# Optimization experiments

Hardware: AMD Instinct MI355X
Metric: run time of the kernel (lower is better)

## Reference

```python
import jax, jax.numpy as jnp
import numpy as np


def setup_inputs() -> dict:
    key = jax.random.key(0)
    k1, k2, k3, k4 = jax.random.split(key, 4)
    n, c, p1, p2, r = 8, 3, 512, 512, 8
    X = jax.random.uniform(k1, (n, c, p1, p2), dtype=jnp.float32)
    S = jax.random.uniform(k2, (c, r), dtype=jnp.float32)
    S = S / (jnp.linalg.norm(S, axis=0, keepdims=True))  # unit-norm columns like S_init
    gamma = jax.random.uniform(k3, (1,), dtype=jnp.float32) * 1e-05
    lam = jax.random.uniform(k4, (1,), dtype=jnp.float32) * 1e-05
    return {"X": X, "S": S, "gamma": gamma, "lam": lam, "n_iter": 2}


def reference(X, S, gamma, lam, n_iter):
    n, c, p1, p2 = X.shape
    p = p1 * p2
    r = S.shape[1]
    Xf = X.reshape(n, c, p)
    gamma = jnp.abs(gamma)
    lam = jnp.abs(lam)
    Dt = jnp.zeros((n, r, p), dtype=X.dtype)
    x0 = jnp.mean(Xf, axis=2, keepdims=True)
    for _ in range(n_iter):
        # ---- D update (proximal gradient) ----
        SDt = jnp.einsum('cr,nrp->ncp', S, Dt)  # S @ Dt
        x0 = jnp.mean(Xf + SDt, axis=2, keepdims=True)  # [n,c,1]
        tau_D = 1.0 / jnp.sum(S * S)  # 1/||S||_F^2
        Dt = Dt - tau_D * jnp.einsum('cr,ncp->nrp', S, SDt + Xf - x0)
        S_nrm = jnp.linalg.norm(S, axis=0).reshape(1, r, 1)  # [1,r,1]
        Dt = jax.nn.relu(Dt - lam * gamma * tau_D * S_nrm)
        Dt_L2 = jnp.linalg.norm(Dt, axis=2, keepdims=True)  # [n,r,1]
        scl = jax.nn.relu(Dt_L2 - lam * tau_D * S_nrm)
        scl = scl / Dt_L2 + 1e-10  # faithful to source (eps added after divide)
        Dt = Dt * scl
        # ---- S update (proximal gradient) ----
        SDt = jnp.einsum('cr,nrp->ncp', S, Dt)
        x0 = jnp.mean(Xf + SDt, axis=2, keepdims=True)
        Dt_sum = jnp.sum(Dt, axis=2, keepdims=True)  # [n,r,1]
        tau_S = 1.0 / jnp.mean(jnp.sum(Dt * Dt, axis=(1, 2)))
        grad = jnp.mean(
            jnp.einsum('ncp,nqp->ncq', SDt + Xf, Dt)
            - x0 @ jnp.transpose(Dt_sum, (0, 2, 1)),
            axis=0)  # [c,r]
        S_grad = S - tau_S * grad
        Dt_nrm = jnp.mean(
            gamma * jnp.sum(jnp.abs(Dt), axis=2, keepdims=True)
            + jnp.linalg.norm(Dt, axis=2, keepdims=True), axis=0)  # [r,1]
        Sg_nrm = jnp.linalg.norm(S_grad, axis=0, keepdims=True)  # [1,r]
        scl_S = jax.nn.relu(Sg_nrm - lam * tau_S * Dt_nrm.T)
        scl_S = scl_S / (Sg_nrm + 1e-10)
        S = S_grad * scl_S
        # ---- unit-norm rescale (unit_norm_S=True) ----
        S_nrm2 = jnp.linalg.norm(S, axis=0, keepdims=True)  # [1,r]
        S = S / (S_nrm2 + 1e-10)
        Dt = Dt * (S_nrm2.reshape(1, r, 1) + 1e-10)
    return x0, S, Dt.reshape(n, r, p1, p2)
```

## Files before the change

kernel.cpp:

```cpp
#include <hip/hip_runtime.h>

constexpr int N = 8, C = 3, R = 8;
constexpr int P = 512 * 512;
constexpr int BLK = 256;
constexpr int NB = 64;
constexpr int PPB = P / NB;
constexpr int PITER = PPB / (BLK * 4);
constexpr int NK = 68;

typedef float f32x4 __attribute__((ext_vector_type(4)));

constexpr int W_XMEAN = 0;
constexpr int W_S1    = 32;
constexpr int W_F1    = 64;
constexpr int W_THR2  = 128;
constexpr int W_TAU2  = 136;
constexpr int W_SNRM2 = 144;
constexpr int W_X02   = 160;
constexpr int W_PXF   = 256;
constexpr int W_PA    = 2048;
constexpr int W_PB    = 36864;

#define XR8(M) M(0) M(1) M(2) M(3) M(4) M(5) M(6) M(7)
#define XTRI(M) \
  M(0,0) \
  M(1,0) M(1,1) \
  M(2,0) M(2,1) M(2,2) \
  M(3,0) M(3,1) M(3,2) M(3,3) \
  M(4,0) M(4,1) M(4,2) M(4,3) M(4,4) \
  M(5,0) M(5,1) M(5,2) M(5,3) M(5,4) M(5,5) \
  M(6,0) M(6,1) M(6,2) M(6,3) M(6,4) M(6,5) M(6,6) \
  M(7,0) M(7,1) M(7,2) M(7,3) M(7,4) M(7,5) M(7,6) M(7,7)
#define XCR(M) \
  M(0,0) M(0,1) M(0,2) M(0,3) M(0,4) M(0,5) M(0,6) M(0,7) \
  M(1,0) M(1,1) M(1,2) M(1,3) M(1,4) M(1,5) M(1,6) M(1,7) \
  M(2,0) M(2,1) M(2,2) M(2,3) M(2,4) M(2,5) M(2,6) M(2,7)

__device__ __forceinline__ float sld(float x) {
    return __uint_as_float(__builtin_amdgcn_readfirstlane(__float_as_uint(x)));
}
__device__ __forceinline__ float waveSum(float v) {
    #pragma unroll
    for (int o = 32; o > 0; o >>= 1) v += __shfl_down(v, o);
    return v;
}

__global__ __launch_bounds__(BLK)
void k_xmean(const float* __restrict__ X, float* __restrict__ ws) {
    int nc = blockIdx.y;
    int t = threadIdx.x;
    size_t base = (size_t)nc * P + (size_t)blockIdx.x * 4096;
    float s = 0.f;
    #pragma unroll
    for (int i = 0; i < 4; ++i) {
        float4 q = *(const float4*)(X + base + (size_t)(i * BLK + t) * 4);
        s += (q.x + q.y) + (q.z + q.w);
    }
    __shared__ float red[4];
    s = waveSum(s);
    int lane = t & 63, wid = t >> 6;
    if (lane == 0) red[wid] = s;
    __syncthreads();
    if (t == 0) ws[W_PXF + nc * 64 + blockIdx.x] = (red[0] + red[1]) + (red[2] + red[3]);
}

template <int IT>
__device__ void t23_math(const float* __restrict__ redL, const float* __restrict__ Sin,
                         const float* __restrict__ ws, float lam_, float gam_,
                         float* oS, float* oF, float* oTH2, float* oTAU2,
                         float* oX02, float* oSN2, float* ox0s) {
    const int t = threadIdx.x;
    __shared__ float sum_[N][R], T_[N][R][R], U_[N][C][R];
    __shared__ float scl_[N][R], L2_[N][R], x0s_[N][C], dtn_[R];
    __shared__ float Scur_[24], grad_[24], snrm_in[8];
    __shared__ float tauS_, tauD_;
    for (int i = t; i < NK * N; i += BLK) {
        int k = i / N, nn = i % N;
        float v = redL[k * N + nn];
        if (k < 8) sum_[nn][k] = v;
        else if (k < 44) {
            int m = k - 8; int q = 0;
            while ((q + 1) * (q + 2) / 2 <= m) ++q;
            int r = m - q * (q + 1) / 2;
            T_[nn][r][q] = v; T_[nn][q][r] = v;
        } else { int m = k - 44; U_[nn][m >> 3][m & 7] = v; }
    }
    if (t < 24) Scur_[t] = IT ? ws[W_S1 + t] : Sin[t];
    if (t == 0) {
        if (IT) tauD_ = ws[W_TAU2];
        else { float s = 0.f; for (int i = 0; i < 24; ++i) s += Sin[i] * Sin[i]; tauD_ = 1.0f / s; }
    }
    if (t < 8) {
        if (IT) snrm_in[t] = ws[W_SNRM2 + t];
        else snrm_in[t] = sqrtf(Sin[t] * Sin[t] + Sin[8 + t] * Sin[8 + t] + Sin[16 + t] * Sin[16 + t]);
    }
    __syncthreads();
    for (int i = t; i < N * C * R; i += BLK) {
        int nn = i / 24, m = i % 24, c = m >> 3, q = m & 7;
        U_[nn][c][q] += ws[W_XMEAN + nn * 3 + c] * sum_[nn][q];
    }
    if (t < 64) {
        int nn = t >> 3, r = t & 7;
        float l2 = sqrtf(T_[nn][r][r]);
        float scl = fmaxf(l2 - lam_ * tauD_ * snrm_in[r], 0.f) / l2 + 1e-10f;
        scl_[nn][r] = scl; L2_[nn][r] = l2;
    }
    __syncthreads();
    if (t == 0) {
        float tot = 0.f;
        for (int nn = 0; nn < N; ++nn)
            for (int r = 0; r < R; ++r)
                tot += scl_[nn][r] * scl_[nn][r] * T_[nn][r][r];
        tauS_ = (float)N / tot;
    }
    if (t < 24) {
        int nn = t / 3, c = t % 3;
        float acc = ws[W_XMEAN + t];
        #pragma unroll
        for (int r = 0; r < R; ++r)
            acc += Scur_[c * R + r] * scl_[nn][r] * sum_[nn][r] * (1.0f / P);
        x0s_[nn][c] = acc;
        if (IT == 1) ox0s[t] = acc;
    }
    if (t >= 32 && t < 40) {
        int r = t - 32;
        float a = 0.f;
        #pragma unroll
        for (int nn = 0; nn < N; ++nn)
            a += scl_[nn][r] * (gam_ * sum_[nn][r] + L2_[nn][r]);
        dtn_[r] = a * (1.0f / N);
    }
    __syncthreads();
    if (t < 24) {
        int c = t / 8, q = t % 8;
        float a = 0.f;
        #pragma unroll
        for (int nn = 0; nn < N; ++nn) {
            float m = U_[nn][c][q];
            #pragma unroll
            for (int r = 0; r < R; ++r)
                m += Scur_[c * R + r] * scl_[nn][r] * T_[nn][r][q];
            a += scl_[nn][q] * (m - x0s_[nn][c] * sum_[nn][q]);
        }
        grad_[t] = a * (1.0f / N);
    }
    __syncthreads();
    if (t == 0) {
        float Sg[24], Sn[24];
        #pragma unroll
        for (int i = 0; i < 24; ++i) Sg[i] = Scur_[i] - tauS_ * grad_[i];
        #pragma unroll
        for (int q = 0; q < 8; ++q) {
            float s2 = 0.f;
            #pragma unroll
            for (int c = 0; c < 3; ++c) s2 += Sg[c * 8 + q] * Sg[c * 8 + q];
            float sgn = sqrtf(s2);
            float s = fmaxf(sgn - lam_ * tauS_ * dtn_[q], 0.f) / (sgn + 1e-10f);
            #pragma unroll
            for (int c = 0; c < 3; ++c) Sn[c * 8 + q] = Sg[c * 8 + q] * s;
        }
        #pragma unroll
        for (int q = 0; q < 8; ++q) {
            float s2 = 0.f;
            #pragma unroll
            for (int c = 0; c < 3; ++c) s2 += Sn[c * 8 + q] * Sn[c * 8 + q];
            float n2 = sqrtf(s2);
            oSN2[q] = n2;
            #pragma unroll
            for (int c = 0; c < 3; ++c) oS[c * 8 + q] = Sn[c * 8 + q] / (n2 + 1e-10f);
        }
        if (IT == 0) {
            float ssq = 0.f;
            #pragma unroll
            for (int i = 0; i < 24; ++i) ssq += oS[i] * oS[i];
            float tau2 = 1.0f / ssq;
            oTAU2[0] = tau2;
            #pragma unroll
            for (int r = 0; r < 8; ++r) {
                float s2 = oS[r] * oS[r] + oS[8 + r] * oS[8 + r] + oS[16 + r] * oS[16 + r];
                oTH2[r] = lam_ * gam_ * tau2 * sqrtf(s2);
            }
        }
    }
    __syncthreads();
    if (t < 64) oF[t] = scl_[t >> 3][t & 7] * (oSN2[t & 7] + 1e-10f);
    __syncthreads();
    if (IT == 0 && t < 24) {
        int nn = t / 3, c = t % 3;
        float acc = ws[W_XMEAN + t];
        #pragma unroll
        for (int r = 0; r < R; ++r)
            acc += oS[c * R + r] * oF[nn * R + r] * sum_[nn][r] * (1.0f / P);
        oX02[t] = acc;
    }
    __syncthreads();
}

template <int MODE>
__global__ __launch_bounds__(BLK, 1)
void k_dpass(const float* __restrict__ X, const float* __restrict__ Sin,
             const float* __restrict__ gp, const float* __restrict__ lp,
             float* __restrict__ ws, const float* __restrict__ part_in,
             float* __restrict__ part_out, float* __restrict__ Dt_out,
             float* __restrict__ x0_out, float* __restrict__ S_out) {
    const int n = blockIdx.y, t = threadIdx.x;

    __shared__ float redL[NK * N];
    __shared__ float oS[24], oF[64], oTH2[8], oTAU2[1], oX02[24], oSN2[8], ox0s[24];
    __shared__ float Lxm[24];
    __shared__ float redE[4 * NK];

    const float lamv = fabsf(*lp), gamv = fabsf(*gp);

    float ssq0 = 0.f;
    #pragma unroll
    for (int i = 0; i < 24; ++i) { float v = Sin[i]; ssq0 = fmaf(v, v, ssq0); }
    const float tau1c = sld(1.0f / ssq0);
#define LD_TH1(r) const float th1_##r = sld(lamv * gamv * tau1c * sqrtf(fmaf(Sin[r], Sin[r], fmaf(Sin[8 + r], Sin[8 + r], Sin[16 + r] * Sin[16 + r]))));
    XR8(LD_TH1)

    if constexpr (MODE == 0) {
        if (t < 24) {
            const float* px = ws + W_PXF + t * 64;
            float s = 0.f;
            #pragma unroll
            for (int j = 0; j < 64; ++j) s += px[j];
            Lxm[t] = s * (1.0f / P);
        }
        __syncthreads();
        if (blockIdx.x == 0 && n == 0 && t < 24) ws[W_XMEAN + t] = Lxm[t];
    } else {
        for (int row = t; row < NK * N; row += BLK) {
            const float* pr = part_in + (size_t)row * NB;
            float s = 0.f;
            #pragma unroll
            for (int j = 0; j < NB / 4; ++j) {
                float4 q = *(const float4*)(pr + j * 4);
                s += (q.x + q.y) + (q.z + q.w);
            }
            redL[row] = s;
        }
        __syncthreads();
        t23_math<(MODE == 1 ? 0 : 1)>(redL, Sin, ws, lamv, gamv,
                                      oS, oF, oTH2, oTAU2, oX02, oSN2, ox0s);
        if constexpr (MODE == 1) {
            if (blockIdx.x == 0 && n == 0) {
                if (t < 24) ws[W_S1 + t] = oS[t];
                if (t < 64) ws[W_F1 + t] = oF[t];
                if (t < 8)  ws[W_THR2 + t] = oTH2[t];
                if (t == 0) ws[W_TAU2] = oTAU2[0];
                if (t < 24) ws[W_X02 + t] = oX02[t];
                if (t < 8)  ws[W_SNRM2 + t] = oSN2[t];
            }
        } else {
            if (blockIdx.x == 0 && n == 0 && t < 24) {
                x0_out[t] = ox0s[t];
                S_out[t] = oS[t];
            }
        }
    }

    const float x01_0 = sld(MODE == 0 ? Lxm[n * 3 + 0] : ws[W_XMEAN + n * 3 + 0]);
    const float x01_1 = sld(MODE == 0 ? Lxm[n * 3 + 1] : ws[W_XMEAN + n * 3 + 1]);
    const float x01_2 = sld(MODE == 0 ? Lxm[n * 3 + 2] : ws[W_XMEAN + n * 3 + 2]);
#define LD_S0(c,q) const float S0_##c##q = sld(Sin[(c) * 8 + (q)]);
    XCR(LD_S0)
#define LD_S1(c,q) const float S1_##c##q = (MODE >= 1) ? sld(MODE == 1 ? oS[(c) * 8 + (q)] : ws[W_S1 + (c) * 8 + (q)]) : 0.f;
    XCR(LD_S1)
#define LD_F1(r)  const float f1_##r = (MODE >= 1) ? sld(MODE == 1 ? oF[n * 8 + (r)] : ws[W_F1 + n * 8 + (r)]) : 0.f;
#define LD_TH2(r) const float th2_##r = (MODE >= 1) ? sld(MODE == 1 ? oTH2[(r)] : ws[W_THR2 + (r)]) : 0.f;
#define LD_F2(r)  const float f2_##r = (MODE == 2) ? sld(oF[n * 8 + (r)]) : 0.f;
    XR8(LD_F1) XR8(LD_TH2) XR8(LD_F2)
    const float tau2c = (MODE >= 1) ? sld(MODE == 1 ? oTAU2[0] : ws[W_TAU2]) : 0.f;
    const float dx0_0 = (MODE >= 1) ? sld(ws[W_XMEAN + n * 3 + 0] - (MODE == 1 ? oX02[n * 3 + 0] : ws[W_X02 + n * 3 + 0])) : 0.f;
    const float dx0_1 = (MODE >= 1) ? sld(ws[W_XMEAN + n * 3 + 1] - (MODE == 1 ? oX02[n * 3 + 1] : ws[W_X02 + n * 3 + 1])) : 0.f;
    const float dx0_2 = (MODE >= 1) ? sld(ws[W_XMEAN + n * 3 + 2] - (MODE == 1 ? oX02[n * 3 + 2] : ws[W_X02 + n * 3 + 2])) : 0.f;

#define D_SM(r)   float sm_##r = 0.f;
#define D_T(q,r)  float tq_##q##_##r = 0.f;
#define D_V(c,q)  float vv_##c##_##q = 0.f;
    XR8(D_SM) XTRI(D_T) XCR(D_V)

    const float* Xn = X + (size_t)n * C * P;
    float* Dn = Dt_out + (size_t)n * R * P;

#define C_P1(r) const float p_##r = fmaxf(fmaf(-tau1c, fmaf(S0_0##r, tt0, fmaf(S0_1##r, tt1, S0_2##r * tt2)), -th1_##r), 0.f);
#define C_AL(r) const float a_##r = p_##r;
#define C_D2(r) const float d_##r = f1_##r * p_##r;
#define C_W(c)  const float w##c = fmaf(S1_##c##0, d_0, fmaf(S1_##c##1, d_1, fmaf(S1_##c##2, d_2, fmaf(S1_##c##3, d_3, fmaf(S1_##c##4, d_4, fmaf(S1_##c##5, d_5, fmaf(S1_##c##6, d_6, fmaf(S1_##c##7, d_7, tt##c + dx0_##c))))))));
#define C_A2(r) const float a_##r = fmaxf(fmaf(-tau2c, fmaf(S1_0##r, w0, fmaf(S1_1##r, w1, S1_2##r * w2)), d_##r - th2_##r), 0.f);
#define AC_SM(r)  sm_##r += a_##r;
#define AC_T(q,r) tq_##q##_##r = fmaf(a_##r, a_##q, tq_##q##_##r);
#define AC_V(c,q) vv_##c##_##q = fmaf(tt##c, a_##q, vv_##c##_##q);
#define PXc(r) ov_##r.x = f2_##r * a_##r;
#define PYc(r) ov_##r.y = f2_##r * a_##r;
#define PZc(r) ov_##r.z = f2_##r * a_##r;
#define PWc(r) ov_##r.w = f2_##r * a_##r;
#define GXc(q) (q).x
#define GYc(q) (q).y
#define GZc(q) (q).z
#define GWc(q) (q).w

#define SITE(GET, PUTM) { \
    const float tt0 = GET(xv0) - x01_0; \
    const float tt1 = GET(xv1) - x01_1; \
    const float tt2 = GET(xv2) - x01_2; \
    XR8(C_P1) \
    if constexpr (MODE == 0) { \
        XR8(C_AL) XR8(AC_SM) XTRI(AC_T) XCR(AC_V) \
    } else { \
        XR8(C_D2) C_W(0) C_W(1) C_W(2) XR8(C_A2) \
        if constexpr (MODE == 1) { XR8(AC_SM) XTRI(AC_T) XCR(AC_V) } \
        else { XR8(PUTM) } \
    } }

#define D_OV(r) float4 ov_##r;
#define ST_O(r) { f32x4 wv = { ov_##r.x, ov_##r.y, ov_##r.z, ov_##r.w }; \
                  __builtin_nontemporal_store(wv, (f32x4*)(Dn + (size_t)(r) * P + pbase)); }

    #pragma unroll
    for (int it = 0; it < PITER; ++it) {
        size_t pbase = (size_t)blockIdx.x * PPB + (size_t)(it * BLK + t) * 4;
        float4 xv0 = *(const float4*)(Xn + 0 * (size_t)P + pbase);
        float4 xv1 = *(const float4*)(Xn + 1 * (size_t)P + pbase);
        float4 xv2 = *(const float4*)(Xn + 2 * (size_t)P + pbase);
        XR8(D_OV)
        SITE(GXc, PXc)
        SITE(GYc, PYc)
        SITE(GZc, PZc)
        SITE(GWc, PWc)
        if constexpr (MODE == 2) { XR8(ST_O) }
    }

    if constexpr (MODE < 2) {
        const int lane = t & 63, wid = t >> 6;
#define RD_SM(r)  { float v = waveSum(sm_##r);       if (lane == 0) redE[wid * NK + (r)] = v; }
#define RD_T(q,r) { float v = waveSum(tq_##q##_##r); if (lane == 0) redE[wid * NK + 8 + (q) * ((q) + 1) / 2 + (r)] = v; }
#define RD_V(c,q) { float v = waveSum(vv_##c##_##q); if (lane == 0) redE[wid * NK + 44 + (c) * R + (q)] = v; }
        XR8(RD_SM) XTRI(RD_T) XCR(RD_V)
        __syncthreads();
        for (int k = t; k < NK; k += BLK)
            part_out[((size_t)k * N + n) * NB + blockIdx.x] =
                (redE[k] + redE[NK + k]) + (redE[2 * NK + k] + redE[3 * NK + k]);
    }
}

extern "C" void kernel_launch(void* const* d_in, const int* in_sizes, int n_in,
                              void* d_out, int out_size, void* d_ws, size_t ws_size,
                              hipStream_t stream) {
    const float* X   = (const float*)d_in[0];
    const float* Sin = (const float*)d_in[1];
    const float* gam = (const float*)d_in[2];
    const float* lam = (const float*)d_in[3];
    float* out    = (float*)d_out;
    float* x0_out = out;
    float* S_out  = out + 24;
    float* Dt_out = out + 48;
    float* ws     = (float*)d_ws;
    float* partA  = ws + W_PA;
    float* partB  = ws + W_PB;

    k_xmean<<<dim3(64, N * C), BLK, 0, stream>>>(X, ws);
    k_dpass<0><<<dim3(NB, N), BLK, 0, stream>>>(X, Sin, gam, lam, ws, partA, partA, Dt_out, x0_out, S_out);
    k_dpass<1><<<dim3(NB, N), BLK, 0, stream>>>(X, Sin, gam, lam, ws, partA, partB, Dt_out, x0_out, S_out);
    k_dpass<2><<<dim3(NB, N), BLK, 0, stream>>>(X, Sin, gam, lam, ws, partB, partA, Dt_out, x0_out, S_out);
}
```

Baseline: 98.40 us.

## Replace partial-sum buffers with atomic accumulation and double block count

Cross-block reductions (the X means and the 68 per-batch statistics) now go through float atomicAdd into a small zeroed workspace instead of per-block partial arrays that every block re-reduced at the start of the next pass. Each block of MODE 2 recomputes the iteration-1 scalar math redundantly rather than reading it back from workspace. The grid doubles to 128 blocks per batch, and the in-block reduction uses quad shuffles plus a padded shared table. This removes the per-block partial re-read, at the cost of atomic contention, a memset launch, nondeterministic summation order and duplicated t23 math in MODE 2.

```diff
diff --git a/kernel.cpp b/kernel.cpp
--- a/kernel.cpp
+++ b/kernel.cpp
@@ -3,23 +3,17 @@
 constexpr int N = 8, C = 3, R = 8;
 constexpr int P = 512 * 512;
 constexpr int BLK = 256;
-constexpr int NB = 64;
+constexpr int NB = 128;
 constexpr int PPB = P / NB;
 constexpr int PITER = PPB / (BLK * 4);
 constexpr int NK = 68;
 
 typedef float f32x4 __attribute__((ext_vector_type(4)));
 
-constexpr int W_XMEAN = 0;
-constexpr int W_S1    = 32;
-constexpr int W_F1    = 64;
-constexpr int W_THR2  = 128;
-constexpr int W_TAU2  = 136;
-constexpr int W_SNRM2 = 144;
-constexpr int W_X02   = 160;
-constexpr int W_PXF   = 256;
-constexpr int W_PA    = 2048;
-constexpr int W_PB    = 36864;
+constexpr int W_XSUM = 0;
+constexpr int W_ACC1 = 32;
+constexpr int W_ACC2 = 608;
+constexpr int W_ZEND = 1152;
 
 #define XR8(M) M(0) M(1) M(2) M(3) M(4) M(5) M(6) M(7)
 #define XTRI(M) \
@@ -61,22 +55,25 @@
     int lane = t & 63, wid = t >> 6;
     if (lane == 0) red[wid] = s;
     __syncthreads();
-    if (t == 0) ws[W_PXF + nc * 64 + blockIdx.x] = (red[0] + red[1]) + (red[2] + red[3]);
+    if (t == 0) atomicAdd(ws + W_XSUM + nc, (red[0] + red[1]) + (red[2] + red[3]));
 }
 
 template <int IT>
-__device__ void t23_math(const float* __restrict__ redL, const float* __restrict__ Sin,
-                         const float* __restrict__ ws, float lam_, float gam_,
+__device__ void t23_math(const float* __restrict__ accG, const float* __restrict__ SinG,
+                         const float* __restrict__ iS, const float* __restrict__ iTau,
+                         const float* __restrict__ iCN, const float* __restrict__ ws,
+                         float lam_, float gam_,
                          float* oS, float* oF, float* oTH2, float* oTAU2,
-                         float* oX02, float* oSN2, float* ox0s) {
+                         float* oCN, float* oX02, float* ox0s) {
     const int t = threadIdx.x;
+    const float invP = 1.0f / (float)P;
     __shared__ float sum_[N][R], T_[N][R][R], U_[N][C][R];
     __shared__ float scl_[N][R], L2_[N][R], x0s_[N][C], dtn_[R];
-    __shared__ float Scur_[24], grad_[24], snrm_in[8];
+    __shared__ float Scur_[24], grad_[24], snrmI[8], pn_[8];
     __shared__ float tauS_, tauD_;
     for (int i = t; i < NK * N; i += BLK) {
         int k = i / N, nn = i % N;
-        float v = redL[k * N + nn];
+        float v = accG[i];
         if (k < 8) sum_[nn][k] = v;
         else if (k < 44) {
             int m = k - 8; int q = 0;
@@ -85,24 +82,24 @@
             T_[nn][r][q] = v; T_[nn][q][r] = v;
         } else { int m = k - 44; U_[nn][m >> 3][m & 7] = v; }
     }
-    if (t < 24) Scur_[t] = IT ? ws[W_S1 + t] : Sin[t];
+    if (t < 24) Scur_[t] = IT ? iS[t] : SinG[t];
     if (t == 0) {
-        if (IT) tauD_ = ws[W_TAU2];
-        else { float s = 0.f; for (int i = 0; i < 24; ++i) s += Sin[i] * Sin[i]; tauD_ = 1.0f / s; }
+        if (IT) tauD_ = iTau[0];
+        else { float s = 0.f; for (int i = 0; i < 24; ++i) s += SinG[i] * SinG[i]; tauD_ = 1.0f / s; }
     }
     if (t < 8) {
-        if (IT) snrm_in[t] = ws[W_SNRM2 + t];
-        else snrm_in[t] = sqrtf(Sin[t] * Sin[t] + Sin[8 + t] * Sin[8 + t] + Sin[16 + t] * Sin[16 + t]);
+        if (IT) snrmI[t] = iCN[t];
+        else snrmI[t] = sqrtf(SinG[t] * SinG[t] + SinG[8 + t] * SinG[8 + t] + SinG[16 + t] * SinG[16 + t]);
     }
     __syncthreads();
     for (int i = t; i < N * C * R; i += BLK) {
         int nn = i / 24, m = i % 24, c = m >> 3, q = m & 7;
-        U_[nn][c][q] += ws[W_XMEAN + nn * 3 + c] * sum_[nn][q];
+        U_[nn][c][q] += ws[W_XSUM + nn * 3 + c] * invP * sum_[nn][q];
     }
     if (t < 64) {
         int nn = t >> 3, r = t & 7;
         float l2 = sqrtf(T_[nn][r][r]);
-        float scl = fmaxf(l2 - lam_ * tauD_ * snrm_in[r], 0.f) / l2 + 1e-10f;
+        float scl = fmaxf(l2 - lam_ * tauD_ * snrmI[r], 0.f) / l2 + 1e-10f;
         scl_[nn][r] = scl; L2_[nn][r] = l2;
     }
     __syncthreads();
@@ -115,10 +112,10 @@
     }
     if (t < 24) {
         int nn = t / 3, c = t % 3;
-        float acc = ws[W_XMEAN + t];
+        float acc = ws[W_XSUM + t] * invP;
         #pragma unroll
         for (int r = 0; r < R; ++r)
-            acc += Scur_[c * R + r] * scl_[nn][r] * sum_[nn][r] * (1.0f / P);
+            acc += Scur_[c * R + r] * scl_[nn][r] * sum_[nn][r] * invP;
         x0s_[nn][c] = acc;
         if (IT == 1) ox0s[t] = acc;
     }
@@ -165,7 +162,7 @@
             #pragma unroll
             for (int c = 0; c < 3; ++c) s2 += Sn[c * 8 + q] * Sn[c * 8 + q];
             float n2 = sqrtf(s2);
-            oSN2[q] = n2;
+            pn_[q] = n2;
             #pragma unroll
             for (int c = 0; c < 3; ++c) oS[c * 8 + q] = Sn[c * 8 + q] / (n2 + 1e-10f);
         }
@@ -177,20 +174,21 @@
             oTAU2[0] = tau2;
             #pragma unroll
             for (int r = 0; r < 8; ++r) {
-                float s2 = oS[r] * oS[r] + oS[8 + r] * oS[8 + r] + oS[16 + r] * oS[16 + r];
-                oTH2[r] = lam_ * gam_ * tau2 * sqrtf(s2);
+                float cn = sqrtf(oS[r] * oS[r] + oS[8 + r] * oS[8 + r] + oS[16 + r] * oS[16 + r]);
+                oCN[r] = cn;
+                oTH2[r] = lam_ * gam_ * tau2 * cn;
             }
         }
     }
     __syncthreads();
-    if (t < 64) oF[t] = scl_[t >> 3][t & 7] * (oSN2[t & 7] + 1e-10f);
+    if (t < 64) oF[t] = scl_[t >> 3][t & 7] * (pn_[t & 7] + 1e-10f);
     __syncthreads();
     if (IT == 0 && t < 24) {
         int nn = t / 3, c = t % 3;
-        float acc = ws[W_XMEAN + t];
+        float acc = ws[W_XSUM + t] * invP;
         #pragma unroll
         for (int r = 0; r < R; ++r)
-            acc += oS[c * R + r] * oF[nn * R + r] * sum_[nn][r] * (1.0f / P);
+            acc += oS[c * R + r] * oF[nn * R + r] * sum_[nn][r] * invP;
         oX02[t] = acc;
     }
     __syncthreads();
@@ -200,17 +198,11 @@
 __global__ __launch_bounds__(BLK, 1)
 void k_dpass(const float* __restrict__ X, const float* __restrict__ Sin,
              const float* __restrict__ gp, const float* __restrict__ lp,
-             float* __restrict__ ws, const float* __restrict__ part_in,
-             float* __restrict__ part_out, float* __restrict__ Dt_out,
+             float* __restrict__ ws, float* __restrict__ Dt_out,
              float* __restrict__ x0_out, float* __restrict__ S_out) {
     const int n = blockIdx.y, t = threadIdx.x;
-
-    __shared__ float redL[NK * N];
-    __shared__ float oS[24], oF[64], oTH2[8], oTAU2[1], oX02[24], oSN2[8], ox0s[24];
-    __shared__ float Lxm[24];
-    __shared__ float redE[4 * NK];
-
     const float lamv = fabsf(*lp), gamv = fabsf(*gp);
+    const float invP = 1.0f / (float)P;
 
     float ssq0 = 0.f;
     #pragma unroll
@@ -219,62 +211,34 @@
 #define LD_TH1(r) const float th1_##r = sld(lamv * gamv * tau1c * sqrtf(fmaf(Sin[r], Sin[r], fmaf(Sin[8 + r], Sin[8 + r], Sin[16 + r] * Sin[16 + r]))));
     XR8(LD_TH1)
 
-    if constexpr (MODE == 0) {
-        if (t < 24) {
-            const float* px = ws + W_PXF + t * 64;
-            float s = 0.f;
-            #pragma unroll
-            for (int j = 0; j < 64; ++j) s += px[j];
-            Lxm[t] = s * (1.0f / P);
-        }
-        __syncthreads();
-        if (blockIdx.x == 0 && n == 0 && t < 24) ws[W_XMEAN + t] = Lxm[t];
-    } else {
-        for (int row = t; row < NK * N; row += BLK) {
-            const float* pr = part_in + (size_t)row * NB;
-            float s = 0.f;
-            #pragma unroll
-            for (int j = 0; j < NB / 4; ++j) {
-                float4 q = *(const float4*)(pr + j * 4);
-                s += (q.x + q.y) + (q.z + q.w);
-            }
-            redL[row] = s;
-        }
-        __syncthreads();
-        t23_math<(MODE == 1 ? 0 : 1)>(redL, Sin, ws, lamv, gamv,
-                                      oS, oF, oTH2, oTAU2, oX02, oSN2, ox0s);
-        if constexpr (MODE == 1) {
-            if (blockIdx.x == 0 && n == 0) {
-                if (t < 24) ws[W_S1 + t] = oS[t];
-                if (t < 64) ws[W_F1 + t] = oF[t];
-                if (t < 8)  ws[W_THR2 + t] = oTH2[t];
-                if (t == 0) ws[W_TAU2] = oTAU2[0];
-                if (t < 24) ws[W_X02 + t] = oX02[t];
-                if (t < 8)  ws[W_SNRM2 + t] = oSN2[t];
-            }
-        } else {
-            if (blockIdx.x == 0 && n == 0 && t < 24) {
-                x0_out[t] = ox0s[t];
-                S_out[t] = oS[t];
-            }
-        }
-    }
-
-    const float x01_0 = sld(MODE == 0 ? Lxm[n * 3 + 0] : ws[W_XMEAN + n * 3 + 0]);
-    const float x01_1 = sld(MODE == 0 ? Lxm[n * 3 + 1] : ws[W_XMEAN + n * 3 + 1]);
-    const float x01_2 = sld(MODE == 0 ? Lxm[n * 3 + 2] : ws[W_XMEAN + n * 3 + 2]);
+    __shared__ float oS[24], oF[64], oTH2[8], oTAU2[1], oCN[8], oX02[24];
+    __shared__ float oS2[24], oF2[64], ox0s[24];
+
+    if constexpr (MODE >= 1) {
+        t23_math<0>(ws + W_ACC1, Sin, nullptr, nullptr, nullptr, ws, lamv, gamv,
+                    oS, oF, oTH2, oTAU2, oCN, oX02, nullptr);
+    }
+    if constexpr (MODE == 2) {
+        t23_math<1>(ws + W_ACC2, nullptr, oS, oTAU2, oCN, ws, lamv, gamv,
+                    oS2, oF2, nullptr, nullptr, nullptr, nullptr, ox0s);
+        if (blockIdx.x == 0 && n == 0 && t < 24) { x0_out[t] = ox0s[t]; S_out[t] = oS2[t]; }
+    }
+
+    const float x01_0 = sld(ws[W_XSUM + n * 3 + 0] * invP);
+    const float x01_1 = sld(ws[W_XSUM + n * 3 + 1] * invP);
+    const float x01_2 = sld(ws[W_XSUM + n * 3 + 2] * invP);
 #define LD_S0(c,q) const float S0_##c##q = sld(Sin[(c) * 8 + (q)]);
     XCR(LD_S0)
-#define LD_S1(c,q) const float S1_##c##q = (MODE >= 1) ? sld(MODE == 1 ? oS[(c) * 8 + (q)] : ws[W_S1 + (c) * 8 + (q)]) : 0.f;
+#define LD_S1(c,q) const float S1_##c##q = (MODE >= 1) ? sld(oS[(c) * 8 + (q)]) : 0.f;
     XCR(LD_S1)
-#define LD_F1(r)  const float f1_##r = (MODE >= 1) ? sld(MODE == 1 ? oF[n * 8 + (r)] : ws[W_F1 + n * 8 + (r)]) : 0.f;
-#define LD_TH2(r) const float th2_##r = (MODE >= 1) ? sld(MODE == 1 ? oTH2[(r)] : ws[W_THR2 + (r)]) : 0.f;
-#define LD_F2(r)  const float f2_##r = (MODE == 2) ? sld(oF[n * 8 + (r)]) : 0.f;
+#define LD_F1(r)  const float f1_##r = (MODE >= 1) ? sld(oF[n * 8 + (r)]) : 0.f;
+#define LD_TH2(r) const float th2_##r = (MODE >= 1) ? sld(oTH2[(r)]) : 0.f;
+#define LD_F2(r)  const float f2_##r = (MODE == 2) ? sld(oF2[n * 8 + (r)]) : 0.f;
     XR8(LD_F1) XR8(LD_TH2) XR8(LD_F2)
-    const float tau2c = (MODE >= 1) ? sld(MODE == 1 ? oTAU2[0] : ws[W_TAU2]) : 0.f;
-    const float dx0_0 = (MODE >= 1) ? sld(ws[W_XMEAN + n * 3 + 0] - (MODE == 1 ? oX02[n * 3 + 0] : ws[W_X02 + n * 3 + 0])) : 0.f;
-    const float dx0_1 = (MODE >= 1) ? sld(ws[W_XMEAN + n * 3 + 1] - (MODE == 1 ? oX02[n * 3 + 1] : ws[W_X02 + n * 3 + 1])) : 0.f;
-    const float dx0_2 = (MODE >= 1) ? sld(ws[W_XMEAN + n * 3 + 2] - (MODE == 1 ? oX02[n * 3 + 2] : ws[W_X02 + n * 3 + 2])) : 0.f;
+    const float tau2c = (MODE >= 1) ? sld(oTAU2[0]) : 0.f;
+    const float dx0_0 = (MODE >= 1) ? sld(x01_0 - oX02[n * 3 + 0]) : 0.f;
+    const float dx0_1 = (MODE >= 1) ? sld(x01_1 - oX02[n * 3 + 1]) : 0.f;
+    const float dx0_2 = (MODE >= 1) ? sld(x01_2 - oX02[n * 3 + 2]) : 0.f;
 
 #define D_SM(r)   float sm_##r = 0.f;
 #define D_T(q,r)  float tq_##q##_##r = 0.f;
@@ -333,15 +297,24 @@
     }
 
     if constexpr (MODE < 2) {
+        __shared__ float redQ[NK][65];
         const int lane = t & 63, wid = t >> 6;
-#define RD_SM(r)  { float v = waveSum(sm_##r);       if (lane == 0) redE[wid * NK + (r)] = v; }
-#define RD_T(q,r) { float v = waveSum(tq_##q##_##r); if (lane == 0) redE[wid * NK + 8 + (q) * ((q) + 1) / 2 + (r)] = v; }
-#define RD_V(c,q) { float v = waveSum(vv_##c##_##q); if (lane == 0) redE[wid * NK + 44 + (c) * R + (q)] = v; }
+        const int quad = lane >> 2, sub = lane & 3;
+#define RQ(k, val) { float v_ = (val); v_ += __shfl_xor(v_, 1); v_ += __shfl_xor(v_, 2); \
+                     if (sub == ((k) & 3)) redQ[k][wid * 16 + quad] = v_; }
+#define RD_SM(r)  RQ((r), sm_##r)
+#define RD_T(q,r) RQ((8 + (q) * ((q) + 1) / 2 + (r)), tq_##q##_##r)
+#define RD_V(c,q) RQ((44 + (c) * 8 + (q)), vv_##c##_##q)
         XR8(RD_SM) XTRI(RD_T) XCR(RD_V)
         __syncthreads();
-        for (int k = t; k < NK; k += BLK)
-            part_out[((size_t)k * N + n) * NB + blockIdx.x] =
-                (redE[k] + redE[NK + k]) + (redE[2 * NK + k] + redE[3 * NK + k]);
+        float* accOut = ws + (MODE == 0 ? W_ACC1 : W_ACC2);
+        if (t < NK) {
+            const float* row = redQ[t];
+            float s = 0.f;
+            #pragma unroll
+            for (int j = 0; j < 64; ++j) s += row[j];
+            atomicAdd(accOut + t * N + n, s);
+        }
     }
 }
 
@@ -357,11 +330,10 @@
     float* S_out  = out + 24;
     float* Dt_out = out + 48;
     float* ws     = (float*)d_ws;
-    float* partA  = ws + W_PA;
-    float* partB  = ws + W_PB;
-
+
+    hipMemsetAsync(ws, 0, W_ZEND * sizeof(float), stream);
     k_xmean<<<dim3(64, N * C), BLK, 0, stream>>>(X, ws);
-    k_dpass<0><<<dim3(NB, N), BLK, 0, stream>>>(X, Sin, gam, lam, ws, partA, partA, Dt_out, x0_out, S_out);
-    k_dpass<1><<<dim3(NB, N), BLK, 0, stream>>>(X, Sin, gam, lam, ws, partA, partB, Dt_out, x0_out, S_out);
-    k_dpass<2><<<dim3(NB, N), BLK, 0, stream>>>(X, Sin, gam, lam, ws, partB, partA, Dt_out, x0_out, S_out);
-}
+    k_dpass<0><<<dim3(NB, N), BLK, 0, stream>>>(X, Sin, gam, lam, ws, Dt_out, x0_out, S_out);
+    k_dpass<1><<<dim3(NB, N), BLK, 0, stream>>>(X, Sin, gam, lam, ws, Dt_out, x0_out, S_out);
+    k_dpass<2><<<dim3(NB, N), BLK, 0, stream>>>(X, Sin, gam, lam, ws, Dt_out, x0_out, S_out);
+}
```

New measurement: 131.7 us. 1.34x slower.
